# Kernel optimization log

Hardware: AMD Instinct MI355X
Metric: run time of the kernel (lower is better)

The kernel has to match this reference:

```python
import jax, jax.numpy as jnp
import numpy as np

IN_CHANNELS = 16
KERNEL_SIZE = 5
STRIDE = 2
PADDING = 2
BATCH = 32
LENGTH = 131072


def setup_inputs() -> dict:
    key = jax.random.key(0)
    k1, k2 = jax.random.split(key)
    x = jax.random.normal(k1, (BATCH, IN_CHANNELS, LENGTH), dtype=jnp.float32)
    agg_weights = jax.random.normal(k2, (IN_CHANNELS, KERNEL_SIZE), dtype=jnp.float32) * (1.0 / KERNEL_SIZE ** 0.5)
    bias = jnp.zeros((IN_CHANNELS,), dtype=jnp.float32)
    return {"x": x, "agg_weights": agg_weights, "bias": bias}


def reference(x, agg_weights, bias):
    # Replication (edge) pad along length
    x_pad = jnp.pad(x, ((0, 0), (0, 0), (PADDING, PADDING)), mode="edge")
    L_pad = x.shape[-1] + 2 * PADDING
    L_out = (L_pad - KERNEL_SIZE) // STRIDE + 1
    # Accumulate logsigmoid(window_k) * w[:, k] over the small kernel dim,
    # avoiding materializing the full [B, C, K, L_out] im2col tensor.
    acc = jnp.zeros(x.shape[:2] + (L_out,), dtype=x.dtype)
    for k in range(KERNEL_SIZE):
        win = jax.lax.slice_in_dim(x_pad, k, k + STRIDE * (L_out - 1) + 1, axis=2)[:, :, ::STRIDE]
        acc = acc + jax.nn.log_sigmoid(win) * agg_weights[None, :, k, None]
    return jnp.tanh(acc + bias[None, :, None])
```

## Files before the change

### kernel.cpp

```cpp
#include <hip/hip_runtime.h>
#include <math.h>

#define L_IN   131072
#define L_OUT  65536
#define NC     16
#define NB     32
#define KSZ    5

#define THREADS 256
#define OPT     8
#define TPR     (L_OUT / OPT)
#define BPR     (TPR / THREADS)

__device__ __forceinline__ float logsig(float x) {
    float t = __expf(-fabsf(x));
    return fminf(x, 0.0f) - __logf(1.0f + t);
}

__device__ __forceinline__ float fast_tanh(float a) {
    float e = __expf(2.0f * a);
    return 1.0f - __fdividef(2.0f, e + 1.0f);
}

__global__ __launch_bounds__(THREADS) void conv_ls_tanh_kernel(
    const float* __restrict__ x, const float* __restrict__ w,
    const float* __restrict__ bias, float* __restrict__ out)
{
    const int bid = blockIdx.x;
    const int row = bid / BPR;
    const int rb  = bid - row * BPR;
    const int c   = row & (NC - 1);
    const int lt  = rb * THREADS + threadIdx.x;

    const float* xr = x + (size_t)row * L_IN;

    const int ibase = 16 * lt - 4;

    float v[24];
    if (lt != 0 && lt != TPR - 1) {
        const float4* p = (const float4*)(xr + ibase);
        #pragma unroll
        for (int q = 0; q < 6; ++q) {
            float4 d = p[q];
            v[4*q+0] = d.x; v[4*q+1] = d.y; v[4*q+2] = d.z; v[4*q+3] = d.w;
        }
    } else {
        #pragma unroll
        for (int j = 0; j < 24; ++j) {
            int g = ibase + j;
            g = min(max(g, 0), L_IN - 1);
            v[j] = xr[g];
        }
    }

    #pragma unroll
    for (int j = 2; j <= 20; ++j) v[j] = logsig(v[j]);

    const float w0 = w[c*KSZ+0], w1 = w[c*KSZ+1], w2 = w[c*KSZ+2],
                w3 = w[c*KSZ+3], w4 = w[c*KSZ+4];
    const float bb = bias[c];

    float o[OPT];
    #pragma unroll
    for (int i = 0; i < OPT; ++i) {
        const int s = 2*i + 2;
        float acc = v[s+0]*w0 + v[s+1]*w1 + v[s+2]*w2 + v[s+3]*w3 + v[s+4]*w4;
        o[i] = fast_tanh(acc + bb);
    }

    float* op = out + (size_t)row * L_OUT + (size_t)OPT * lt;
    ((float4*)op)[0] = make_float4(o[0], o[1], o[2], o[3]);
    ((float4*)op)[1] = make_float4(o[4], o[5], o[6], o[7]);
}

extern "C" void kernel_launch(void* const* d_in, const int* in_sizes, int n_in,
                              void* d_out, int out_size, void* d_ws, size_t ws_size,
                              hipStream_t stream) {
    const float* x    = (const float*)d_in[0];
    const float* w    = (const float*)d_in[1];
    const float* bias = (const float*)d_in[2];
    float* out        = (float*)d_out;

    const int grid = NB * NC * BPR;
    conv_ls_tanh_kernel<<<grid, THREADS, 0, stream>>>(x, w, bias, out);
}
```

Before: 389.2 us.

## Use coalesced float4 loads with wavefront shuffles for halo exchange

Each thread now loads four coalesced float4 chunks, strided across the block, instead of a contiguous overlapping 24-element window. Neighbouring logsigmoid values come from lane shuffles, so each input is loaded and transformed once rather than with halo overlap. Lanes at wavefront edges reload halo values from global memory, which adds a few scalar loads and divergence. Output stores shrink from two float4 writes to float2 writes per chunk.

```diff
diff --git a/kernel.cpp b/kernel.cpp
--- a/kernel.cpp
+++ b/kernel.cpp
@@ -8,9 +8,10 @@
 #define KSZ    5
 
 #define THREADS 256
-#define OPT     8
-#define TPR     (L_OUT / OPT)
-#define BPR     (TPR / THREADS)
+#define CHUNKS  4
+#define IN_PER_BLOCK  (THREADS * CHUNKS * 4)
+#define OUT_PER_BLOCK (IN_PER_BLOCK / 2)
+#define BPR (L_OUT / OUT_PER_BLOCK)
 
 __device__ __forceinline__ float logsig(float x) {
     float t = __expf(-fabsf(x));
@@ -26,51 +27,56 @@
     const float* __restrict__ x, const float* __restrict__ w,
     const float* __restrict__ bias, float* __restrict__ out)
 {
-    const int bid = blockIdx.x;
-    const int row = bid / BPR;
-    const int rb  = bid - row * BPR;
-    const int c   = row & (NC - 1);
-    const int lt  = rb * THREADS + threadIdx.x;
+    const int bid  = blockIdx.x;
+    const int row  = bid / BPR;
+    const int rb   = bid - row * BPR;
+    const int c    = row & (NC - 1);
+    const int tid  = threadIdx.x;
+    const int lane = tid & 63;
 
-    const float* xr = x + (size_t)row * L_IN;
+    const float* xr   = x   + (size_t)row * L_IN;
+    float*       outr = out + (size_t)row * L_OUT;
 
-    const int ibase = 16 * lt - 4;
-
-    float v[24];
-    if (lt != 0 && lt != TPR - 1) {
-        const float4* p = (const float4*)(xr + ibase);
-        #pragma unroll
-        for (int q = 0; q < 6; ++q) {
-            float4 d = p[q];
-            v[4*q+0] = d.x; v[4*q+1] = d.y; v[4*q+2] = d.z; v[4*q+3] = d.w;
-        }
-    } else {
-        #pragma unroll
-        for (int j = 0; j < 24; ++j) {
-            int g = ibase + j;
-            g = min(max(g, 0), L_IN - 1);
-            v[j] = xr[g];
-        }
-    }
-
-    #pragma unroll
-    for (int j = 2; j <= 20; ++j) v[j] = logsig(v[j]);
+    const int in_base = rb * IN_PER_BLOCK;
 
     const float w0 = w[c*KSZ+0], w1 = w[c*KSZ+1], w2 = w[c*KSZ+2],
                 w3 = w[c*KSZ+3], w4 = w[c*KSZ+4];
     const float bb = bias[c];
 
-    float o[OPT];
+    float4 d[CHUNKS];
     #pragma unroll
-    for (int i = 0; i < OPT; ++i) {
-        const int s = 2*i + 2;
-        float acc = v[s+0]*w0 + v[s+1]*w1 + v[s+2]*w2 + v[s+3]*w3 + v[s+4]*w4;
-        o[i] = fast_tanh(acc + bb);
+    for (int q = 0; q < CHUNKS; ++q) {
+        const int gi = in_base + ((q * THREADS + tid) << 2);
+        d[q] = *(const float4*)(xr + gi);
     }
 
-    float* op = out + (size_t)row * L_OUT + (size_t)OPT * lt;
-    ((float4*)op)[0] = make_float4(o[0], o[1], o[2], o[3]);
-    ((float4*)op)[1] = make_float4(o[4], o[5], o[6], o[7]);
+    #pragma unroll
+    for (int q = 0; q < CHUNKS; ++q) {
+        const int gi = in_base + ((q * THREADS + tid) << 2);
+
+        const float a0 = logsig(d[q].x);
+        const float a1 = logsig(d[q].y);
+        const float a2 = logsig(d[q].z);
+        const float a3 = logsig(d[q].w);
+
+        float lm2 = __shfl_up(a2, 1);
+        float lm1 = __shfl_up(a3, 1);
+        float lp4 = __shfl_down(a0, 1);
+
+        if (lane == 0) {
+            lm2 = logsig(xr[max(gi - 2, 0)]);
+            lm1 = logsig(xr[max(gi - 1, 0)]);
+        }
+        if (lane == 63) {
+            lp4 = logsig(xr[min(gi + 4, L_IN - 1)]);
+        }
+
+        const float o0 = lm2*w0 + lm1*w1 + a0*w2 + a1*w3 + a2*w4;
+        const float o1 = a0*w0  + a1*w1  + a2*w2 + a3*w3 + lp4*w4;
+
+        const int ob = gi >> 1;
+        *(float2*)(outr + ob) = make_float2(fast_tanh(o0 + bb), fast_tanh(o1 + bb));
+    }
 }
 
 extern "C" void kernel_launch(void* const* d_in, const int* in_sizes, int n_in,
```

Measured after the change: 394.4 us. About the same (+1.3%).
